# Optimization experiments

Measured on AMD Instinct MI355X. Metric: run time of the kernel, lower is better.

Reference implementation:

```python
import math
import jax, jax.numpy as jnp
import numpy as np

BLOCK = 32          # MRA block size (fixed to 32 by the CUDA kernels)
NUM_HEADS = 12
HEAD_DIM = 64
NUM_BLOCKS = 512    # top-k blocks kept per (batch*head) row
FIRST_N = 0         # initial_prior_first_n_blocks
DIAG_N = 3          # initial_prior_diagonal_n_blocks


def _low_res_logit(q, k, v, mask):
    # q,k,v: (B, S, D); mask: (B, S)
    B, S, D = q.shape
    nb = S // BLOCK
    tc = mask.reshape(B, nb, BLOCK).sum(-1)            # token count per block
    denom = tc[:, :, None] + 1e-6
    q_hat = q.reshape(B, nb, BLOCK, D).sum(2) / denom
    k_hat = k.reshape(B, nb, BLOCK, D).sum(2) / denom
    v_hat = v.reshape(B, nb, BLOCK, D).sum(2) / denom
    logit = jnp.einsum('bnd,bmd->bnm', q_hat, k_hat) / math.sqrt(D)
    row_max = logit.max(-1, keepdims=True)             # before mask penalty, as in torch
    logit = logit - 1e4 * ((tc[:, None, :] * tc[:, :, None]) < 0.5).astype(logit.dtype)
    return logit, tc, row_max, v_hat


def _block_idxes(lrl):
    # lrl: (B, nb, nb) normalized low-res logits (stop-gradient'ed by caller)
    B, nb, _ = lrl.shape
    if DIAG_N > 0:
        off = DIAG_N // 2
        r = jnp.arange(nb)
        diag = (jnp.abs(r[:, None] - r[None, :]) <= off).astype(lrl.dtype)
        lrl = lrl + diag[None] * 5000.0
    if FIRST_N > 0:
        lrl = lrl.at[:, :FIRST_N, :].add(5000.0)
        lrl = lrl.at[:, :, :FIRST_N].add(5000.0)
    vals, idx = jax.lax.top_k(lrl.reshape(B, -1), NUM_BLOCKS)
    thresh = vals.min(-1)
    hi_mask = (lrl >= thresh[:, None, None]).astype(lrl.dtype)
    return idx, hi_mask


def mra2_attention(q, k, v, mask):
    # q,k,v: (meta_batch, S, D); mask: (meta_batch, S). approx_mode == 'full'.
    B, S, D = q.shape
    nb = S // BLOCK
    q = q * mask[:, :, None]
    k = k * mask[:, :, None]
    v = v * mask[:, :, None]
    lrl, tc, row_max, v_hat = _low_res_logit(q, k, v, mask)
    idx, hi_mask = _block_idxes(jax.lax.stop_gradient(lrl - row_max))
    qi = idx // nb                                     # (B, NUM_BLOCKS) query block id
    ki = idx % nb                                      # (B, NUM_BLOCKS) key block id
    b_ix = jnp.arange(B)[:, None]
    # mm_to_sparse: gather blocks, block layout is (key_pos, query_pos) as in the CUDA kernel
    qb = q.reshape(B, nb, BLOCK, D)[b_ix, qi]          # (B, NB, 32, D)
    kb = k.reshape(B, nb, BLOCK, D)[b_ix, ki]
    hr_logit = jnp.einsum('bnkd,bnqd->bnkq', kb, qb) / math.sqrt(D)
    # sparse_max: per-query-row max over all selected blocks in that row
    idx_vals = hr_logit.max(-2)                        # (B, NB, 32q)
    max_vals = jnp.full((B, nb, BLOCK), -1e9, hr_logit.dtype).at[b_ix, qi].max(idx_vals)
    hr_logit = hr_logit - max_vals[b_ix, qi][:, :, None, :]
    # sparse_mask over key positions of each selected block
    mk = mask.reshape(B, nb, BLOCK)[b_ix, ki]          # (B, NB, 32k)
    hr_logit = hr_logit - 1e4 * (1.0 - mk)[:, :, :, None]
    hr_attn = jnp.exp(hr_logit)
    # sparse_dense_mm: scatter-add block contributions back to query rows
    vb = v.reshape(B, nb, BLOCK, D)[b_ix, ki]
    out_blk = jnp.einsum('bnkq,bnkd->bnqd', hr_attn, vb)
    hr_out = jnp.zeros((B, nb, BLOCK, D), q.dtype).at[b_ix, qi].add(out_blk).reshape(B, S, D)
    hr_norm = jnp.zeros((B, nb, BLOCK), q.dtype).at[b_ix, qi].add(hr_attn.sum(-2)).reshape(B, S)
    max_vals_flat = max_vals.reshape(B, S)
    # low-resolution branch (approx_mode == 'full')
    lr_attn = jnp.exp(lrl - row_max - 1e4 * hi_mask) * tc[:, None, :]
    lr_out = jnp.broadcast_to(
        jnp.einsum('bnm,bmd->bnd', lr_attn, v_hat)[:, :, None, :], (B, nb, BLOCK, D)
    ).reshape(B, S, D)
    lr_norm = jnp.broadcast_to(lr_attn.sum(-1)[:, :, None], (B, nb, BLOCK)).reshape(B, S)
    log_corr = (jnp.broadcast_to(row_max, (B, nb, BLOCK)).reshape(B, S) - max_vals_flat) * mask
    lr_corr = jnp.exp(log_corr * (log_corr <= 0).astype(log_corr.dtype))
    hr_corr = jnp.exp(-log_corr * (log_corr > 0).astype(log_corr.dtype))
    num = hr_out * hr_corr[:, :, None] + lr_out * lr_corr[:, :, None]
    den = hr_norm * hr_corr + lr_norm * lr_corr + 1e-6
    ctx = num / den[:, :, None]
    return ctx * mask[:, :, None]


def setup_inputs() -> dict:
    key = jax.random.key(0)
    ks = jax.random.split(key, 4)
    B, S, H = 4, 4096, 768
    return {
        'hidden_states': jax.random.normal(ks[0], (B, S, H), jnp.float32),
        'attention_mask': jnp.zeros((B, S), jnp.float32),  # extended mask form (0 == keep)
        'Wq': jax.random.normal(ks[1], (H, H), jnp.float32) * 0.02,
        'bq': jnp.zeros((H,), jnp.float32),
        'Wk': jax.random.normal(ks[2], (H, H), jnp.float32) * 0.02,
        'bk': jnp.zeros((H,), jnp.float32),
        'Wv': jax.random.normal(ks[3], (H, H), jnp.float32) * 0.02,
        'bv': jnp.zeros((H,), jnp.float32),
    }


def reference(hidden_states, attention_mask, Wq, bq, Wk, bk, Wv, bv):
    B, S, H = hidden_states.shape

    def heads(x):  # (B,S,H) -> (B*nh, S, hd)
        return x.reshape(B, S, NUM_HEADS, HEAD_DIM).transpose(0, 2, 1, 3).reshape(B * NUM_HEADS, S, HEAD_DIM)

    q = heads(hidden_states @ Wq.T + bq)
    k = heads(hidden_states @ Wk.T + bk)
    v = heads(hidden_states @ Wv.T + bv)
    # revert get_extended_attention_mask: (1 - m) * -10000 -> m
    mask = 1.0 + attention_mask / 10000.0
    mask = jnp.broadcast_to(mask[:, None, :], (B, NUM_HEADS, S)).reshape(B * NUM_HEADS, S)
    ctx = mra2_attention(q, k, v, mask)
    return ctx.reshape(B, NUM_HEADS, S, HEAD_DIM).transpose(0, 2, 1, 3).reshape(B, S, H)
```

## Files before the change

kernel.cpp:

```cpp
#include <hip/hip_runtime.h>
#include <math.h>


#define S_LEN 4096
#define NBLK  128
#define BHT   48
#define HD    64

typedef __attribute__((ext_vector_type(8))) short bf16x8;
typedef __attribute__((ext_vector_type(4))) float f32x4;
typedef unsigned short u16;
typedef unsigned int   u32;
typedef unsigned long long u64;

__device__ __forceinline__ u16 bf16rne(float x) {
    u32 u = __float_as_uint(x);
    u32 r = u + 0x7FFFu + ((u >> 16) & 1u);
    return (u16)(r >> 16);
}
__device__ __forceinline__ float b2f(u16 h) {
    return __uint_as_float((u32)h << 16);
}

__device__ __forceinline__ void gload_lds16(const void* g, void* l) {
    __builtin_amdgcn_global_load_lds((const __attribute__((address_space(1))) void*)g,
                                     (__attribute__((address_space(3))) void*)l, 16, 0, 0);
}

#define NX8 (16384 * 768 / 8)
#define NW8 (768 * 768 / 8)

__global__ __launch_bounds__(256) void split_all(
    const float* __restrict__ X,
    const float* __restrict__ Wq, const float* __restrict__ Wk, const float* __restrict__ Wv,
    u16* __restrict__ Xh, u16* __restrict__ Xl,
    u16* __restrict__ Wh, u16* __restrict__ Wl)
{
    int i = blockIdx.x * 256 + threadIdx.x;
    if (i >= NX8 + 3 * NW8) return;
    const float* src; u16* dh; u16* dl; size_t off8;
    if (i < NX8) { src = X; dh = Xh; dl = Xl; off8 = i; }
    else {
        int j = i - NX8;
        int w = j / NW8, r = j - w * NW8;
        src = (w == 0) ? Wq : (w == 1) ? Wk : Wv;
        dh = Wh + (size_t)w * 768 * 768;
        dl = Wl + (size_t)w * 768 * 768;
        off8 = r;
    }
    const float4* xp = (const float4*)src + off8 * 2;
    float4 a = xp[0], b = xp[1];
    float xs[8] = {a.x, a.y, a.z, a.w, b.x, b.y, b.z, b.w};
    bf16x8 vh, vl;
    #pragma unroll
    for (int j = 0; j < 8; ++j) {
        u16 hh = bf16rne(xs[j]);
        float hf = b2f(hh);
        vh[j] = (short)hh;
        vl[j] = (short)bf16rne(xs[j] - hf);
    }
    *(bf16x8*)&dh[off8 * 8] = vh;
    *(bf16x8*)&dl[off8 * 8] = vl;
}

__global__ __launch_bounds__(256, 3) void qkv_mfma(
    const u16* __restrict__ Xh, const u16* __restrict__ Xl,
    const u16* __restrict__ Wh, const u16* __restrict__ Wl,
    const float* __restrict__ bq, const float* __restrict__ bk, const float* __restrict__ bv,
    const float* __restrict__ am,
    u16* __restrict__ Qh, u16* __restrict__ Ql,
    u16* __restrict__ Kh, u16* __restrict__ Kl,
    u16* __restrict__ Vth, u16* __restrict__ Vtl)
{
    const int wg = blockIdx.x;
    const int logical = (wg & 7) * 288 + (wg >> 3);
    const int z   = logical / 768;
    const int idx = logical - z * 768;
    const int mt  = idx / 6;
    const int nt  = idx - mt * 6;

    const float* bias = (z == 0) ? bq : (z == 1) ? bk : bv;
    const u16* Wzh = Wh + (size_t)z * 768 * 768;
    const u16* Wzl = Wl + (size_t)z * 768 * 768;
    const int m0 = mt * 128, n0 = nt * 128;

    __shared__ char smem[32768];
    const int tid  = threadIdx.x;
    const int lane = tid & 63;
    const int w    = tid >> 6;
    const int wm   = (w >> 1) * 64, wn = (w & 1) * 64;

    const int rbase = (w < 2) ? m0 : n0;
    const int sub0  = (w & 1) * 4;
    char* ldsdst    = (w < 2) ? smem : (smem + 16384);
    const int srow = lane >> 2;
    const int scg  = (lane & 3) ^ ((lane >> 3) & 3);
    const int tslot = (lane & 15) * 4 + ((lane >> 4) ^ ((lane >> 1) & 3));

    f32x4 acc[4][4];
    #pragma unroll
    for (int i = 0; i < 4; ++i)
        #pragma unroll
        for (int j = 0; j < 4; ++j) acc[i][j] = (f32x4){0.f, 0.f, 0.f, 0.f};

    for (int k0 = 0; k0 < 2304; k0 += 64) {
        const u16* srcA = (k0 < 1536) ? Xh : Xl;
        const u16* srcB = (k0 < 768) ? Wzh : ((k0 < 1536) ? Wzl : Wzh);
        const int  kk   = (k0 < 768) ? k0 : ((k0 < 1536) ? (k0 - 768) : (k0 - 1536));
        const u16* src  = (w < 2) ? srcA : srcB;
        __syncthreads();
        #pragma unroll
        for (int h = 0; h < 2; ++h)
            #pragma unroll
            for (int i = 0; i < 4; ++i) {
                int sub = sub0 + i;
                const u16* g = src + (size_t)(rbase + sub * 16 + srow) * 768
                                   + (kk + h * 32 + scg * 8);
                gload_lds16(g, ldsdst + (h * 8 + sub) * 1024);
            }
        __syncthreads();

        #pragma unroll
        for (int h = 0; h < 2; ++h) {
            bf16x8 af[4], bf[4];
            #pragma unroll
            for (int f = 0; f < 4; ++f) {
                af[f] = *(const bf16x8*)&smem[(h * 8 + (w >> 1) * 4 + f) * 1024 + tslot * 16];
                bf[f] = *(const bf16x8*)&smem[16384 + (h * 8 + (w & 1) * 4 + f) * 1024 + tslot * 16];
            }
            #pragma unroll
            for (int i = 0; i < 4; ++i)
                #pragma unroll
                for (int j = 0; j < 4; ++j)
                    acc[i][j] = __builtin_amdgcn_mfma_f32_16x16x32_bf16(af[i], bf[j], acc[i][j], 0, 0, 0);
        }
    }

    if (z < 2) {
        u16* Ph = (z == 0) ? Qh : Kh;
        u16* Pl = (z == 0) ? Ql : Kl;
        const float qscale = (z == 0) ? 0.125f : 1.0f;
        #pragma unroll
        for (int i = 0; i < 4; ++i) {
            #pragma unroll
            for (int j = 0; j < 4; ++j) {
                int col = n0 + wn + j * 16 + (lane & 15);
                int h = col >> 6, d = col & 63;
                float bsv = bias[col];
                #pragma unroll
                for (int r = 0; r < 4; ++r) {
                    int row = m0 + wm + i * 16 + (lane >> 4) * 4 + r;
                    int b = row >> 12, s = row & 4095;
                    float mv = 1.0f + am[row] * 1e-4f;
                    float e = (acc[i][j][r] + bsv) * mv * qscale;
                    u16 hh = bf16rne(e);
                    u16 ll = bf16rne(e - b2f(hh));
                    size_t a = (((size_t)(b * 12 + h)) * S_LEN + s) * HD + d;
                    Ph[a] = hh; Pl[a] = ll;
                }
            }
        }
    } else {
        u32* buf = (u32*)smem;
        const int bb = m0 >> 12;
        #pragma unroll
        for (int p = 0; p < 4; ++p) {
            const int hh_ = p & 1;
            const int rh  = p >> 1;
            __syncthreads();
            if (((w & 1) == hh_) && ((w >> 1) == rh)) {
                #pragma unroll
                for (int i = 0; i < 4; ++i) {
                    #pragma unroll
                    for (int j = 0; j < 4; ++j) {
                        int d_local = j * 16 + (lane & 15);
                        int col = n0 + hh_ * 64 + d_local;
                        float bsv = bias[col];
                        #pragma unroll
                        for (int r = 0; r < 4; ++r) {
                            int s_local = i * 16 + (lane >> 4) * 4 + r;
                            float mv = 1.0f + am[m0 + rh * 64 + s_local] * 1e-4f;
                            float e = (acc[i][j][r] + bsv) * mv;
                            u16 h16 = bf16rne(e);
                            u16 l16 = bf16rne(e - b2f(h16));
                            buf[d_local * 66 + s_local] = ((u32)h16 << 16) | (u32)l16;
                        }
                    }
                }
            }
            __syncthreads();
            int d_local = tid >> 2;
            int s_chunk = (tid & 3) * 16;
            int head = (n0 >> 6) + hh_;
            size_t ob = (((size_t)(bb * 12 + head)) * HD + d_local) * S_LEN
                        + (m0 & 4095) + rh * 64 + s_chunk;
            #pragma unroll
            for (int gq = 0; gq < 2; ++gq) {
                bf16x8 vh8, vl8;
                #pragma unroll
                for (int t = 0; t < 8; ++t) {
                    u32 pk = buf[d_local * 66 + s_chunk + gq * 8 + t];
                    vh8[t] = (short)(pk >> 16);
                    vl8[t] = (short)(pk & 0xFFFF);
                }
                *(bf16x8*)&Vth[ob + gq * 8] = vh8;
                *(bf16x8*)&Vtl[ob + gq * 8] = vl8;
            }
        }
    }
}

__global__ __launch_bounds__(256) void hsum_kernel(
    const float* __restrict__ X, const float* __restrict__ am,
    double* __restrict__ hsum, double* __restrict__ tcd)
{
    int blk = blockIdx.x & 127, b = blockIdx.x >> 7;
    int tid = threadIdx.x;
    const float* xb  = X  + ((size_t)(b * S_LEN + blk * 32)) * 768;
    const float* amb = am + b * S_LEN + blk * 32;
    for (int d = tid; d < 768; d += 256) {
        double s = 0.0;
        for (int t = 0; t < 32; ++t)
            s += (double)xb[(size_t)t * 768 + d] * (1.0 + (double)amb[t] * 1e-4);
        hsum[(size_t)blockIdx.x * 768 + d] = s;
    }
    if (tid == 0) {
        double t = 0.0;
        for (int i = 0; i < 32; ++i) t += 1.0 + (double)amb[i] * 1e-4;
        tcd[blockIdx.x] = t;
    }
}

__global__ __launch_bounds__(256) void ghat_kernel(
    const double* __restrict__ hsum,
    const float* __restrict__ Wq, const float* __restrict__ Wk,
    const float* __restrict__ bq, const float* __restrict__ bk,
    const double* __restrict__ tcd,
    double* __restrict__ qhat, double* __restrict__ khat)
{
    const float* W; const float* bias; double* outp;
    if (blockIdx.z == 0) { W = Wq; bias = bq; outp = qhat; }
    else                 { W = Wk; bias = bk; outp = khat; }
    const int n0 = blockIdx.x * 64, m0 = blockIdx.y * 64;
    __shared__ double As[16][72];
    __shared__ float  Bs[16][72];
    const int tid = threadIdx.x;
    const int tx = tid & 15, ty = tid >> 4;
    double acc[4][4] = {};
    const int lr = tid >> 2, lc = (tid & 3) * 4;
    for (int k0 = 0; k0 < 768; k0 += 16) {
        double a0 = hsum[(size_t)(m0 + lr) * 768 + k0 + lc + 0];
        double a1 = hsum[(size_t)(m0 + lr) * 768 + k0 + lc + 1];
        double a2 = hsum[(size_t)(m0 + lr) * 768 + k0 + lc + 2];
        double a3 = hsum[(size_t)(m0 + lr) * 768 + k0 + lc + 3];
        float4 bv = *(const float4*)&W[(size_t)(n0 + lr) * 768 + k0 + lc];
        __syncthreads();
        As[lc+0][lr] = a0; As[lc+1][lr] = a1; As[lc+2][lr] = a2; As[lc+3][lr] = a3;
        Bs[lc+0][lr] = bv.x; Bs[lc+1][lr] = bv.y; Bs[lc+2][lr] = bv.z; Bs[lc+3][lr] = bv.w;
        __syncthreads();
        #pragma unroll
        for (int kk = 0; kk < 16; ++kk) {
            double af[4]; float bf[4];
            #pragma unroll
            for (int i = 0; i < 4; ++i) af[i] = As[kk][ty*4+i];
            #pragma unroll
            for (int j = 0; j < 4; ++j) bf[j] = Bs[kk][tx*4+j];
            #pragma unroll
            for (int i = 0; i < 4; ++i)
                #pragma unroll
                for (int j = 0; j < 4; ++j)
                    acc[i][j] += af[i] * (double)bf[j];
        }
    }
    #pragma unroll
    for (int i = 0; i < 4; ++i) {
        int m = m0 + ty*4 + i;
        int b = m >> 7, blk = m & 127;
        double t = tcd[m];
        #pragma unroll
        for (int j = 0; j < 4; ++j) {
            int o = n0 + tx*4 + j;
            int h = o >> 6, d = o & 63;
            outp[(((size_t)(b*12 + h)) * NBLK + blk) * HD + d] = (acc[i][j] + t * (double)bias[o]) / (t + 1e-6);
        }
    }
}

__global__ __launch_bounds__(128) void lrl_kernel(
    const double* __restrict__ qhat, const double* __restrict__ khat,
    const double* __restrict__ tcd,
    double* __restrict__ lrl, double* __restrict__ rmax,
    u64* __restrict__ keys)
{
    const int q0 = blockIdx.x * 4, bh = blockIdx.y;
    const int b = bh / 12;
    __shared__ double qr[4][64];
    __shared__ double red[4][128];
    const int tid = threadIdx.x;
    if (tid < 64) {
        #pragma unroll
        for (int qq = 0; qq < 4; ++qq)
            qr[qq][tid] = qhat[(((size_t)bh) * NBLK + q0 + qq) * HD + tid];
    }
    __syncthreads();
    const double* kr = &khat[(((size_t)bh) * NBLK + tid) * HD];
    double s[4] = {0.0, 0.0, 0.0, 0.0};
    for (int d = 0; d < 64; d += 2) {
        double2 kv2 = *(const double2*)&kr[d];
        #pragma unroll
        for (int qq = 0; qq < 4; ++qq)
            s[qq] += qr[qq][d] * kv2.x + qr[qq][d + 1] * kv2.y;
    }
    #pragma unroll
    for (int qq = 0; qq < 4; ++qq) { s[qq] *= 0.125; red[qq][tid] = s[qq]; }
    __syncthreads();
    for (int off = 64; off > 0; off >>= 1) {
        if (tid < off) {
            #pragma unroll
            for (int qq = 0; qq < 4; ++qq)
                red[qq][tid] = fmax(red[qq][tid], red[qq][tid + off]);
        }
        __syncthreads();
    }
    const double tck = tcd[b * NBLK + tid];
    #pragma unroll
    for (int qq = 0; qq < 4; ++qq) {
        const int qi = q0 + qq;
        const double rmaxv = red[qq][0];
        double pen = (tcd[b * NBLK + qi] * tck < 0.5) ? 1e4 : 0.0;
        const double lv = s[qq] - pen;
        lrl[(size_t)bh * (NBLK*NBLK) + (size_t)qi * NBLK + tid] = lv;
        if (tid == 0) rmax[bh * NBLK + qi] = rmaxv;
        int dd = qi - tid; if (dd < 0) dd = -dd;
        double ks_ = lv - rmaxv + ((dd <= 1) ? 5000.0 : 0.0);
        u64 u = (u64)__double_as_longlong(ks_);
        u = (u >> 63) ? ~u : (u | 0x8000000000000000ULL);
        keys[(size_t)bh * (NBLK*NBLK) + (size_t)qi * NBLK + tid] = u;
    }
}

__global__ __launch_bounds__(64) void vhat_kernel(
    const u16* __restrict__ Vth, const u16* __restrict__ Vtl,
    const double* __restrict__ tcd,
    float* __restrict__ vhat, float* __restrict__ tcf)
{
    const int d = blockIdx.x, bh = blockIdx.y;
    const int b = bh / 12;
    const int l = threadIdx.x;
    const u16* ph = Vth + ((size_t)bh * HD + d) * S_LEN + l * 64;
    const u16* pl = Vtl + ((size_t)bh * HD + d) * S_LEN + l * 64;
    float s[2] = {0.f, 0.f};
    #pragma unroll
    for (int g = 0; g < 2; ++g) {
        #pragma unroll
        for (int v = 0; v < 4; ++v) {
            bf16x8 vh = *(const bf16x8*)&ph[g * 32 + v * 8];
            bf16x8 vl = *(const bf16x8*)&pl[g * 32 + v * 8];
            #pragma unroll
            for (int j = 0; j < 8; ++j)
                s[g] += b2f((u16)vh[j]) + b2f((u16)vl[j]);
        }
    }
    #pragma unroll
    for (int g = 0; g < 2; ++g) {
        int blk = l * 2 + g;
        float tc = (float)tcd[b * NBLK + blk];
        vhat[(((size_t)bh) * NBLK + blk) * HD + d] = s[g] / (tc + 1e-6f);
        if (d == 0) tcf[bh * NBLK + blk] = tc;
    }
}

__global__ __launch_bounds__(256) void topk_kernel(
    const u64* __restrict__ keys,
    double* __restrict__ th64, int* __restrict__ cnt, unsigned char* __restrict__ lists,
    int* __restrict__ eqbuf, int* __restrict__ eqcnt)
{
    const int bh = blockIdx.x, tid = threadIdx.x;
    const int wid = tid >> 6;
    __shared__ int hist[4][256];
    __shared__ u64 s_pref;
    __shared__ int s_K;
    const u64* kp = keys + (size_t)bh * (NBLK*NBLK);
    if (tid < 128) cnt[bh * NBLK + tid] = 0;
    if (tid == 0) eqcnt[bh] = 0;

    u64 pref = 0, pmask = 0;
    int K = 512;
    for (int by = 7; by >= 0; --by) {
        #pragma unroll
        for (int w = 0; w < 4; ++w) hist[w][tid] = 0;
        __syncthreads();
        for (int i = tid; i < NBLK*NBLK; i += 256) {
            u64 u = kp[i];
            if ((u & pmask) == pref)
                atomicAdd(&hist[wid][(int)((u >> (by*8)) & 255)], 1);
        }
        __syncthreads();
        int tot = hist[0][tid] + hist[1][tid] + hist[2][tid] + hist[3][tid];
        hist[0][tid] = tot;
        __syncthreads();
        if (tid == 0) {
            int c = 0, bsel = 0;
            for (int x = 255; x >= 0; --x) {
                if (c + hist[0][x] >= K) { bsel = x; break; }
                c += hist[0][x];
            }
            s_pref = pref | ((u64)bsel << (by*8));
            s_K = K - c;
        }
        __syncthreads();
        pref = s_pref; K = s_K;
        pmask |= 0xFFULL << (by*8);
        __syncthreads();
    }
    const u64 tkey = pref;
    int n_take = K;
    if (tid == 0) {
        u64 u = (tkey & 0x8000000000000000ULL) ? (tkey ^ 0x8000000000000000ULL) : ~tkey;
        th64[bh] = __longlong_as_double((long long)u);
    }
    for (int i = tid; i < NBLK*NBLK; i += 256) {
        u64 u = kp[i];
        if (u > tkey) {
            int qi = i >> 7, ki = i & 127;
            int pos = atomicAdd(&cnt[bh * NBLK + qi], 1);
            lists[(((size_t)bh) * NBLK + qi) * NBLK + pos] = (unsigned char)ki;
        } else if (u == tkey) {
            int e = atomicAdd(&eqcnt[bh], 1);
            if (e < 512) eqbuf[bh * 512 + e] = i;
        }
    }
    __syncthreads();
    if (tid == 0) {
        int ne = eqcnt[bh]; if (ne > 512) ne = 512;
        int* eb = &eqbuf[bh * 512];
        for (int a = 1; a < ne; ++a) {
            int v = eb[a]; int x = a - 1;
            while (x >= 0 && eb[x] > v) { eb[x+1] = eb[x]; --x; }
            eb[x+1] = v;
        }
        if (n_take > ne) n_take = ne;
        for (int j = 0; j < n_take; ++j) {
            int i = eb[j]; int qi = i >> 7, ki = i & 127;
            int pos = cnt[bh * NBLK + qi]++;
            lists[(((size_t)bh) * NBLK + qi) * NBLK + pos] = (unsigned char)ki;
        }
    }
    __syncthreads();
    if (tid < 128) {
        int n = cnt[bh * NBLK + tid];
        unsigned char* l = &lists[(((size_t)bh) * NBLK + tid) * NBLK];
        for (int a = 1; a < n; ++a) {
            unsigned char v = l[a]; int x = a - 1;
            while (x >= 0 && l[x] > v) { l[x+1] = l[x]; --x; }
            l[x+1] = v;
        }
    }
}

__global__ __launch_bounds__(64) void hr_mfma(
    const u16* __restrict__ Qh, const u16* __restrict__ Ql,
    const u16* __restrict__ Kh, const u16* __restrict__ Kl,
    const u16* __restrict__ Vth, const u16* __restrict__ Vtl,
    const double* __restrict__ lrl64, const double* __restrict__ rmax64, const double* __restrict__ th64,
    const int* __restrict__ cnt, const unsigned char* __restrict__ lists,
    const float* __restrict__ vhat, const float* __restrict__ tcf,
    const float* __restrict__ am, float* __restrict__ out)
{
    const int qi = blockIdx.x, bh = blockIdx.y;
    const int l  = threadIdx.x;
    const int lr_ = l & 15, lg = l >> 4;
    __shared__ u16 PhL[2][32][40];
    __shared__ u16 PlL[2][32][40];
    __shared__ float wlr[128];
    __shared__ float lrvec[64];

    bf16x8 qfh[2][2], qfl[2][2];
    #pragma unroll
    for (int qs = 0; qs < 2; ++qs)
        #pragma unroll
        for (int ds = 0; ds < 2; ++ds) {
            size_t a = (((size_t)bh) * S_LEN + qi * 32 + qs * 16 + lr_) * HD + ds * 32 + lg * 8;
            qfh[qs][ds] = *(const bf16x8*)&Qh[a];
            qfl[qs][ds] = *(const bf16x8*)&Ql[a];
        }

    float m_run[2][4], l_part[2][4];
    f32x4 oacc[2][4];
    #pragma unroll
    for (int qs = 0; qs < 2; ++qs) {
        #pragma unroll
        for (int r = 0; r < 4; ++r) { m_run[qs][r] = -1e30f; l_part[qs][r] = 0.f; }
        #pragma unroll
        for (int dv = 0; dv < 4; ++dv) oacc[qs][dv] = (f32x4){0.f, 0.f, 0.f, 0.f};
    }

    const int c = cnt[bh * NBLK + qi];
    const unsigned char* ml = &lists[(((size_t)bh) * NBLK + qi) * NBLK];

    int pb = 0;
    for (int bi = 0; bi < c; ++bi) {
        const int ki = ml[bi];
        f32x4 S[2][2];
        #pragma unroll
        for (int qs = 0; qs < 2; ++qs)
            #pragma unroll
            for (int ks = 0; ks < 2; ++ks) S[qs][ks] = (f32x4){0.f, 0.f, 0.f, 0.f};
        #pragma unroll
        for (int ds = 0; ds < 2; ++ds)
            #pragma unroll
            for (int ks = 0; ks < 2; ++ks) {
                size_t a = (((size_t)bh) * S_LEN + ki * 32 + ks * 16 + lr_) * HD + ds * 32 + lg * 8;
                bf16x8 kh = *(const bf16x8*)&Kh[a];
                bf16x8 kl = *(const bf16x8*)&Kl[a];
                S[0][ks] = __builtin_amdgcn_mfma_f32_16x16x32_bf16(qfh[0][ds], kh, S[0][ks], 0, 0, 0);
                S[1][ks] = __builtin_amdgcn_mfma_f32_16x16x32_bf16(qfh[1][ds], kh, S[1][ks], 0, 0, 0);
                S[0][ks] = __builtin_amdgcn_mfma_f32_16x16x32_bf16(qfh[0][ds], kl, S[0][ks], 0, 0, 0);
                S[1][ks] = __builtin_amdgcn_mfma_f32_16x16x32_bf16(qfh[1][ds], kl, S[1][ks], 0, 0, 0);
                S[0][ks] = __builtin_amdgcn_mfma_f32_16x16x32_bf16(qfl[0][ds], kh, S[0][ks], 0, 0, 0);
                S[1][ks] = __builtin_amdgcn_mfma_f32_16x16x32_bf16(qfl[1][ds], kh, S[1][ks], 0, 0, 0);
            }
        float lmax[2][4];
        bool need = false;
        #pragma unroll
        for (int qs = 0; qs < 2; ++qs)
            #pragma unroll
            for (int r = 0; r < 4; ++r) {
                lmax[qs][r] = fmaxf(S[qs][0][r], S[qs][1][r]);
                need |= (lmax[qs][r] > m_run[qs][r] + 8.f);
            }
        if (__any(need)) {
            #pragma unroll
            for (int qs = 0; qs < 2; ++qs)
                #pragma unroll
                for (int r = 0; r < 4; ++r) {
                    float bm = lmax[qs][r];
                    bm = fmaxf(bm, __shfl_xor(bm, 1));
                    bm = fmaxf(bm, __shfl_xor(bm, 2));
                    bm = fmaxf(bm, __shfl_xor(bm, 4));
                    bm = fmaxf(bm, __shfl_xor(bm, 8));
                    float mn = fmaxf(m_run[qs][r], bm);
                    float sc = __expf(m_run[qs][r] - mn);
                    m_run[qs][r] = mn;
                    l_part[qs][r] *= sc;
                    #pragma unroll
                    for (int dv = 0; dv < 4; ++dv) oacc[qs][dv][r] *= sc;
                }
        }
        #pragma unroll
        for (int qs = 0; qs < 2; ++qs)
            #pragma unroll
            for (int r = 0; r < 4; ++r) {
                float p0 = __expf(S[qs][0][r] - m_run[qs][r]);
                float p1 = __expf(S[qs][1][r] - m_run[qs][r]);
                l_part[qs][r] += p0 + p1;
                int row = qs * 16 + lg * 4 + r;
                u16 h0 = bf16rne(p0); u16 lo0 = bf16rne(p0 - b2f(h0));
                u16 h1 = bf16rne(p1); u16 lo1 = bf16rne(p1 - b2f(h1));
                PhL[pb][row][lr_]      = h0;  PlL[pb][row][lr_]      = lo0;
                PhL[pb][row][16 + lr_] = h1;  PlL[pb][row][16 + lr_] = lo1;
            }
        __syncthreads();
        bf16x8 pah[2], pal[2];
        #pragma unroll
        for (int qs = 0; qs < 2; ++qs) {
            pah[qs] = *(const bf16x8*)&PhL[pb][qs * 16 + lr_][lg * 8];
            pal[qs] = *(const bf16x8*)&PlL[pb][qs * 16 + lr_][lg * 8];
        }
        #pragma unroll
        for (int dv = 0; dv < 4; ++dv) {
            size_t a = (((size_t)bh) * HD + dv * 16 + lr_) * S_LEN + ki * 32 + lg * 8;
            bf16x8 vh = *(const bf16x8*)&Vth[a];
            bf16x8 vl = *(const bf16x8*)&Vtl[a];
            #pragma unroll
            for (int qs = 0; qs < 2; ++qs) {
                oacc[qs][dv] = __builtin_amdgcn_mfma_f32_16x16x32_bf16(pah[qs], vh, oacc[qs][dv], 0, 0, 0);
                oacc[qs][dv] = __builtin_amdgcn_mfma_f32_16x16x32_bf16(pah[qs], vl, oacc[qs][dv], 0, 0, 0);
                oacc[qs][dv] = __builtin_amdgcn_mfma_f32_16x16x32_bf16(pal[qs], vh, oacc[qs][dv], 0, 0, 0);
            }
        }
        pb ^= 1;
    }
    __syncthreads();

    float l_run[2][4];
    #pragma unroll
    for (int qs = 0; qs < 2; ++qs)
        #pragma unroll
        for (int r = 0; r < 4; ++r) {
            float rs = l_part[qs][r];
            rs += __shfl_xor(rs, 1);
            rs += __shfl_xor(rs, 2);
            rs += __shfl_xor(rs, 4);
            rs += __shfl_xor(rs, 8);
            l_run[qs][r] = rs;
        }

    const double thv  = th64[bh];
    const double rm64 = rmax64[bh * NBLK + qi];
    const int b = bh / 12, h = bh % 12;
    float wpair = 0.f;
    #pragma unroll
    for (int half = 0; half < 2; ++half) {
        int m = l + half * 64;
        double lv = lrl64[(size_t)bh * (NBLK*NBLK) + (size_t)qi * NBLK + m];
        int dd = qi - m; if (dd < 0) dd = -dd;
        double s = lv - rm64 + ((dd <= 1) ? 5000.0 : 0.0);
        float wv;
        if (s >= thv) wv = 0.f;
        else          wv = (float)exp(lv - rm64) * tcf[bh * NBLK + m];
        wlr[m] = wv;
        wpair += wv;
    }
    float s_lrn = wpair;
    s_lrn += __shfl_xor(s_lrn, 1);
    s_lrn += __shfl_xor(s_lrn, 2);
    s_lrn += __shfl_xor(s_lrn, 4);
    s_lrn += __shfl_xor(s_lrn, 8);
    s_lrn += __shfl_xor(s_lrn, 16);
    s_lrn += __shfl_xor(s_lrn, 32);
    __syncthreads();
    float a_ = 0.f;
    for (int m = 0; m < 128; ++m)
        a_ += wlr[m] * vhat[(((size_t)bh) * NBLK + m) * HD + l];
    lrvec[l] = a_;
    __syncthreads();
    float lv4[4];
    #pragma unroll
    for (int dv = 0; dv < 4; ++dv) lv4[dv] = lrvec[dv * 16 + lr_];

    const float rmf = (float)rm64;
    #pragma unroll
    for (int qs = 0; qs < 2; ++qs)
        #pragma unroll
        for (int r = 0; r < 4; ++r) {
            int q = qs * 16 + lg * 4 + r;
            int srow = qi * 32 + q;
            float mv = 1.0f + am[b * S_LEN + srow] * 1e-4f;
            float logc = (rmf - m_run[qs][r]) * mv;
            float lrc = (logc <= 0.f) ? expf(logc)  : 1.0f;
            float hrc = (logc >  0.f) ? expf(-logc) : 1.0f;
            float den = l_run[qs][r] * hrc + s_lrn * lrc + 1e-6f;
            float scd = mv / den;
            size_t ob = ((size_t)(b * S_LEN + srow)) * 768 + h * HD;
            #pragma unroll
            for (int dv = 0; dv < 4; ++dv)
                out[ob + dv * 16 + lr_] = (oacc[qs][dv][r] * hrc + lv4[dv] * lrc) * scd;
        }
}

extern "C" void kernel_launch(void* const* d_in, const int* in_sizes, int n_in,
                              void* d_out, int out_size, void* d_ws, size_t ws_size,
                              hipStream_t stream)
{
    (void)in_sizes; (void)n_in; (void)out_size; (void)ws_size;
    const float* X  = (const float*)d_in[0];
    const float* am = (const float*)d_in[1];
    const float* Wq = (const float*)d_in[2];
    const float* bq = (const float*)d_in[3];
    const float* Wk = (const float*)d_in[4];
    const float* bk = (const float*)d_in[5];
    const float* Wv = (const float*)d_in[6];
    const float* bv = (const float*)d_in[7];
    float* out = (float*)d_out;

    char* p = (char*)d_ws;
    const size_t PLANE = (size_t)BHT * S_LEN * HD * 2;
    u16* Qh  = (u16*)p; p += PLANE;
    u16* Ql  = (u16*)p; p += PLANE;
    u16* Kh  = (u16*)p; p += PLANE;
    u16* Kl  = (u16*)p; p += PLANE;
    u16* Vth = (u16*)p; p += PLANE;
    u16* Vtl = (u16*)p; p += PLANE;
    char* region = p;

    char* pa = region;
    u16* Xh = (u16*)pa; pa += (size_t)16384 * 768 * 2;
    u16* Xl = (u16*)pa; pa += (size_t)16384 * 768 * 2;
    u16* Wh = (u16*)pa; pa += (size_t)3 * 768 * 768 * 2;
    u16* Wl = (u16*)pa; pa += (size_t)3 * 768 * 768 * 2;

    char* pb = region;
    double* hsum   = (double*)pb; pb += (size_t)512 * 768 * 8;
    double* tcd    = (double*)pb; pb += (size_t)512 * 8;
    double* qhat64 = (double*)pb; pb += (size_t)BHT * NBLK * HD * 8;
    double* khat64 = (double*)pb; pb += (size_t)BHT * NBLK * HD * 8;
    double* lrl64  = (double*)pb; pb += (size_t)BHT * NBLK * NBLK * 8;
    double* rmax64 = (double*)pb; pb += (size_t)BHT * NBLK * 8;
    double* th64   = (double*)pb; pb += (size_t)BHT * 8;
    u64* keys   = (u64*)pb;   pb += (size_t)BHT * NBLK * NBLK * 8;
    float* vhat = (float*)pb; pb += (size_t)BHT * NBLK * HD * 4;
    float* tcf  = (float*)pb; pb += (size_t)BHT * NBLK * 4;
    int* cnt    = (int*)pb;   pb += (size_t)BHT * NBLK * 4;
    int* eqbuf  = (int*)pb;   pb += (size_t)BHT * 512 * 4;
    int* eqcnt  = (int*)pb;   pb += (size_t)BHT * 4;
    unsigned char* lists = (unsigned char*)pb; pb += (size_t)BHT * NBLK * NBLK;

    split_all<<<7008, 256, 0, stream>>>(X, Wq, Wk, Wv, Xh, Xl, Wh, Wl);
    qkv_mfma<<<2304, 256, 0, stream>>>(Xh, Xl, Wh, Wl, bq, bk, bv, am,
                                       Qh, Ql, Kh, Kl, Vth, Vtl);

    hsum_kernel<<<512, 256, 0, stream>>>(X, am, hsum, tcd);
    ghat_kernel<<<dim3(12, 8, 2), 256, 0, stream>>>(hsum, Wq, Wk, bq, bk, tcd, qhat64, khat64);
    lrl_kernel<<<dim3(32, BHT), 128, 0, stream>>>(qhat64, khat64, tcd, lrl64, rmax64, keys);
    vhat_kernel<<<dim3(64, BHT), 64, 0, stream>>>(Vth, Vtl, tcd, vhat, tcf);
    topk_kernel<<<BHT, 256, 0, stream>>>(keys, th64, cnt, lists, eqbuf, eqcnt);

    hr_mfma<<<dim3(NBLK, BHT), 64, 0, stream>>>(Qh, Ql, Kh, Kl, Vth, Vtl,
                                                lrl64, rmax64, th64,
                                                cnt, lists, vhat, tcf, am, out);
}
```

Baseline: 639.7 us.

## Triple-buffer LDS staging in QKV projection GEMM with async prefetch

Rewrites the QKV projection GEMM main loop as a three-stage LDS ring with K-step 32. Global-to-LDS loads for step t+2 are issued while step t is computed, and explicit vmcnt waits replace the two full __syncthreads per iteration. The aim is to overlap memory latency with MFMA work and reduce barrier stalls. In exchange it uses 48KB of LDS, which may lower occupancy, and runs twice as many loop iterations, each with a barrier.

Result: slower. 856.4 us (+33.9%).

```diff
diff --git a/kernel.cpp b/kernel.cpp
--- a/kernel.cpp
+++ b/kernel.cpp
@@ -84,7 +84,7 @@
     const u16* Wzl = Wl + (size_t)z * 768 * 768;
     const int m0 = mt * 128, n0 = nt * 128;
 
-    __shared__ char smem[32768];
+    __shared__ char smem[49152];
     const int tid  = threadIdx.x;
     const int lane = tid & 63;
     const int w    = tid >> 6;
@@ -92,7 +92,6 @@
 
     const int rbase = (w < 2) ? m0 : n0;
     const int sub0  = (w & 1) * 4;
-    char* ldsdst    = (w < 2) ? smem : (smem + 16384);
     const int srow = lane >> 2;
     const int scg  = (lane & 3) ^ ((lane >> 3) & 3);
     const int tslot = (lane & 15) * 4 + ((lane >> 4) ^ ((lane >> 1) & 3));
@@ -103,38 +102,47 @@
         #pragma unroll
         for (int j = 0; j < 4; ++j) acc[i][j] = (f32x4){0.f, 0.f, 0.f, 0.f};
 
-    for (int k0 = 0; k0 < 2304; k0 += 64) {
+    auto STAGE = [&](int buf, int t) {
+        const int k0 = t * 32;
         const u16* srcA = (k0 < 1536) ? Xh : Xl;
         const u16* srcB = (k0 < 768) ? Wzh : ((k0 < 1536) ? Wzl : Wzh);
         const int  kk   = (k0 < 768) ? k0 : ((k0 < 1536) ? (k0 - 768) : (k0 - 1536));
         const u16* src  = (w < 2) ? srcA : srcB;
-        __syncthreads();
-        #pragma unroll
-        for (int h = 0; h < 2; ++h)
-            #pragma unroll
-            for (int i = 0; i < 4; ++i) {
-                int sub = sub0 + i;
-                const u16* g = src + (size_t)(rbase + sub * 16 + srow) * 768
-                                   + (kk + h * 32 + scg * 8);
-                gload_lds16(g, ldsdst + (h * 8 + sub) * 1024);
-            }
-        __syncthreads();
-
-        #pragma unroll
-        for (int h = 0; h < 2; ++h) {
-            bf16x8 af[4], bf[4];
-            #pragma unroll
-            for (int f = 0; f < 4; ++f) {
-                af[f] = *(const bf16x8*)&smem[(h * 8 + (w >> 1) * 4 + f) * 1024 + tslot * 16];
-                bf[f] = *(const bf16x8*)&smem[16384 + (h * 8 + (w & 1) * 4 + f) * 1024 + tslot * 16];
-            }
-            #pragma unroll
-            for (int i = 0; i < 4; ++i)
-                #pragma unroll
-                for (int j = 0; j < 4; ++j)
-                    acc[i][j] = __builtin_amdgcn_mfma_f32_16x16x32_bf16(af[i], bf[j], acc[i][j], 0, 0, 0);
-        }
-    }
+        char* dst = smem + buf * 16384 + ((w < 2) ? 0 : 8192);
+        #pragma unroll
+        for (int i = 0; i < 4; ++i) {
+            const u16* g = src + (size_t)(rbase + (sub0 + i) * 16 + srow) * 768 + (kk + scg * 8);
+            gload_lds16(g, dst + (sub0 + i) * 1024);
+        }
+    };
+
+    STAGE(0, 0);
+    STAGE(1, 1);
+    int cb = 0;
+    for (int t = 0; t < 72; ++t) {
+        if (t == 71) { asm volatile("s_waitcnt vmcnt(0)" ::: "memory"); }
+        else         { asm volatile("s_waitcnt vmcnt(4)" ::: "memory"); }
+        __builtin_amdgcn_s_barrier();
+        __builtin_amdgcn_sched_barrier(0);
+        if (t + 2 < 72) {
+            int sb = (cb + 2 >= 3) ? (cb - 1) : (cb + 2);
+            STAGE(sb, t + 2);
+        }
+        const char* bufp = smem + cb * 16384;
+        bf16x8 af[4], bf[4];
+        #pragma unroll
+        for (int f = 0; f < 4; ++f) {
+            af[f] = *(const bf16x8*)&bufp[((w >> 1) * 4 + f) * 1024 + tslot * 16];
+            bf[f] = *(const bf16x8*)&bufp[8192 + ((w & 1) * 4 + f) * 1024 + tslot * 16];
+        }
+        #pragma unroll
+        for (int i = 0; i < 4; ++i)
+            #pragma unroll
+            for (int j = 0; j < 4; ++j)
+                acc[i][j] = __builtin_amdgcn_mfma_f32_16x16x32_bf16(af[i], bf[j], acc[i][j], 0, 0, 0);
+        cb = (cb == 2) ? 0 : (cb + 1);
+    }
+    __syncthreads();
 
     if (z < 2) {
         u16* Ph = (z == 0) ? Qh : Kh;
```
